# Performance work log

Hardware: AMD Instinct MI355X
Metric: run time of the kernel (lower is better)

The kernel has to match this reference:

```python
import jax, jax.numpy as jnp
import numpy as np

EPS = 1e-3   # Keras BatchNormalization default epsilon
DT = 0.2     # dt
K = 2        # PDE time steps


def _bn(x, p):
    # p: [4, C] = (gamma, beta, moving_mean, moving_var); inference-mode BN
    g, b, m, v = p
    return g * (x - m) * jax.lax.rsqrt(v + EPS) + b


def _dw(x, k):
    # depthwise 3x3 'same' conv; x: NHWC, k: (3,3,1,C)
    return jax.lax.conv_general_dilated(
        x, k, window_strides=(1, 1), padding='SAME',
        dimension_numbers=('NHWC', 'HWIO', 'NHWC'),
        feature_group_count=x.shape[-1])


def setup_inputs() -> dict:
    key = jax.random.key(0)
    ks = jax.random.split(key, 10)
    B, H, W, C = 16, 128, 128, 64
    x = jax.random.normal(ks[0], (B, H, W, C), jnp.float32)

    def kern(k):
        return jax.random.normal(k, (3, 3, 1, C), jnp.float32) * 0.1

    def bnp(k):
        k1, k2, k3, k4 = jax.random.split(k, 4)
        return jnp.stack([
            1.0 + 0.1 * jax.random.normal(k1, (C,), jnp.float32),  # gamma
            0.1 * jax.random.normal(k2, (C,), jnp.float32),        # beta
            0.1 * jax.random.normal(k3, (C,), jnp.float32),        # moving_mean
            0.5 + jax.random.uniform(k4, (C,), jnp.float32),       # moving_var > 0
        ])

    return {
        's0': x,
        'kg': kern(ks[1]), 'kg1': kern(ks[2]),
        'kDx': kern(ks[3]), 'kDy': kern(ks[4]),
        'bng': bnp(ks[5]), 'bng1': bnp(ks[6]),
        'bnDx': bnp(ks[7]), 'bnDy': bnp(ks[8]),
        'bn_out': bnp(ks[9]),
    }


def reference(s0, kg, kg1, kDx, kDy, bng, bng1, bnDx, bnDy, bn_out):
    # init_h is identity ('default' block_type); stride==1, in_chs==out_chs
    f = s0
    h = f
    h0 = f
    g = jax.nn.relu(_bn(_dw(h, kg), bng))
    g1 = jax.nn.relu(_bn(_dw(h, kg1), bng1))
    Dx = jax.nn.relu(_bn(_dw(h, kDx), bnDx))
    Dy = jax.nn.relu(_bn(_dw(h, kDy), bnDy))
    # dx = dy = 1; rolls on axis 2 and 3 exactly as in the TF code (NHWC)
    ux = 0.5 * (jnp.roll(g, 1, axis=2) - jnp.roll(g, -1, axis=2))
    vy = 0.5 * (jnp.roll(g1, 1, axis=3) - jnp.roll(g1, -1, axis=3))
    Ax = g * DT
    Ay = g1 * DT
    Bx = Dx * DT
    By = Dy * DT
    E = (ux + vy) * DT
    D = 1.0 / (1.0 + 2.0 * Bx + 2.0 * By)
    for _ in range(K):
        prev_h = h
        h = D * ((1.0 - 2.0 * Bx - 2.0 * By) * h0
                 - 2.0 * E * h
                 + (-Ax + 2.0 * Bx) * jnp.roll(h, 1, axis=2)
                 + (Ax + 2.0 * Bx) * jnp.roll(h, -1, axis=2)
                 + (-Ay + 2.0 * By) * jnp.roll(h, 1, axis=3)
                 + (Ay + 2.0 * By) * jnp.roll(h, -1, axis=3))
        h = h + D * (2.0 * DT) * f
        h0 = prev_h
    return jax.nn.relu(_bn(h, bn_out))
```

## Files before the change

### kernel.cpp

```cpp
#include <hip/hip_runtime.h>

#define HH 128
#define WW 128
#define CC 64
#define BS 512
#define RS (WW * CC)
#define NPT 4
#define NSTRIP 32
#define ROWS 8

typedef float f4 __attribute__((ext_vector_type(4)));

static __device__ __forceinline__ f4 vload(const float* p) {
    return *reinterpret_cast<const f4*>(p);
}
static __device__ __forceinline__ void vstore(float* p, f4 v) {
    *reinterpret_cast<f4*>(p) = v;
}
static __device__ __forceinline__ f4 vrelu(f4 a) {
    f4 r;
    #pragma unroll
    for (int i = 0; i < 4; ++i) r[i] = fmaxf(a[i], 0.f);
    return r;
}
static __device__ __forceinline__ f4 vrsq_eps(f4 a) {
    f4 r;
    #pragma unroll
    for (int i = 0; i < 4; ++i) r[i] = __builtin_amdgcn_rsqf(a[i] + 1e-3f);
    return r;
}
static __device__ __forceinline__ f4 vrcp(f4 a) {
    f4 r;
    #pragma unroll
    for (int i = 0; i < 4; ++i) r[i] = __builtin_amdgcn_rcpf(a[i]);
    return r;
}
static __device__ __forceinline__ void croll(f4 v, int lm, int lp, f4& cm, f4& cp) {
    const float m3 = __shfl(v.w, lm);
    const float p0 = __shfl(v.x, lp);
    cm.x = m3;  cm.y = v.x; cm.z = v.y; cm.w = v.z;
    cp.x = v.y; cp.y = v.z; cp.z = v.w; cp.w = p0;
}

static __device__ __forceinline__ void gld_lds16(const float* g, float* l) {
    __builtin_amdgcn_global_load_lds(
        (const __attribute__((address_space(1))) void*)g,
        (__attribute__((address_space(3))) void*)l,
        16, 0, 0);
}
static __device__ __forceinline__ void stage_row(const float* g, float* l,
                                                 int wv, int ln) {
    #pragma unroll
    for (int it = 0; it < 4; ++it) {
        const int off = (it * 8 + wv) * 256;
        gld_lds16(g + off + ln * 4, l + off);
    }
}

template<bool CENTER>
static __device__ __forceinline__ void conv_taps(
    const float* R, const float* WTS, int kbase, const int* oc,
    bool zl, bool zr, int c4,
    f4* ag, f4* ag1, f4* adx, f4* ady, f4* h)
{
    f4 in[6];
    #pragma unroll
    for (int jj = 0; jj < 6; ++jj) in[jj] = vload(R + oc[jj]);
    if (zl) in[0] = (f4)0.f;
    if (zr) in[5] = (f4)0.f;
    if (CENTER) {
        #pragma unroll
        for (int i = 0; i < NPT; ++i) h[i] = in[i + 1];
    }
    #pragma unroll
    for (int dw = 0; dw < 3; ++dw) {
        const int kk = kbase + dw;
        const f4 wg  = vload(WTS + (0 * 9 + kk) * CC + c4);
        const f4 wg1 = vload(WTS + (1 * 9 + kk) * CC + c4);
        const f4 wdx = vload(WTS + (2 * 9 + kk) * CC + c4);
        const f4 wdy = vload(WTS + (3 * 9 + kk) * CC + c4);
        #pragma unroll
        for (int i = 0; i < NPT; ++i) {
            ag[i]  += in[dw + i] * wg;
            ag1[i] += in[dw + i] * wg1;
            adx[i] += in[dw + i] * wdx;
            ady[i] += in[dw + i] * wdy;
        }
    }
}

__global__ __launch_bounds__(BS) void diffusion_fused(
    const float* __restrict__ s0,
    const float* __restrict__ kg,  const float* __restrict__ kg1,
    const float* __restrict__ kDx, const float* __restrict__ kDy,
    const float* __restrict__ bng,  const float* __restrict__ bng1,
    const float* __restrict__ bnDx, const float* __restrict__ bnDy,
    const float* __restrict__ bn_out,
    float* __restrict__ out)
{
    __shared__ __attribute__((aligned(16))) float ring[3][RS];
    __shared__ __attribute__((aligned(16))) float GH[2 * NSTRIP * CC];
    __shared__ __attribute__((aligned(16))) float HHb[2 * NSTRIP * CC];
    __shared__ __attribute__((aligned(16))) float WTS[4 * 9 * CC];
    __shared__ __attribute__((aligned(16))) float BNF[10 * CC];

    const int t  = threadIdx.x;
    const int cq = t & 15;
    const int c4 = cq << 2;
    const int s  = t >> 4;
    const int w0 = s << 2;
    const int l  = t & 63;
    const int wv = t >> 6;
    const int lm = (l & 48) | ((l + 15) & 15);
    const int lp = (l & 48) | ((l + 1)  & 15);
    const int sl = (s + NSTRIP - 1) & (NSTRIP - 1);
    const int sr = (s + 1) & (NSTRIP - 1);

    const int bid = blockIdx.x;
    const int img = bid >> 4;
    const int r0  = (bid & 15) << 3;
    const long imgbase = (long)img * HH * RS;

    const bool zl = (s == 0), zr = (s == NSTRIP - 1);
    int oc[6];
    oc[0] = (zl ? 0 : (w0 - 1)) * CC + c4;
    #pragma unroll
    for (int j = 1; j <= 4; ++j) oc[j] = (w0 + j - 1) * CC + c4;
    oc[5] = (zr ? (WW - 1) : (w0 + 4)) * CC + c4;
    const int wmo = ((w0 - 1) & (WW - 1)) * CC + c4;
    const int wpo = ((w0 + 4) & (WW - 1)) * CC + c4;

    if (r0 > 0)
        stage_row(s0 + imgbase + (long)(r0 - 1) * RS, ring[(r0 - 1) % 3], wv, l);
    stage_row(s0 + imgbase + (long)r0 * RS,       ring[r0 % 3],       wv, l);
    stage_row(s0 + imgbase + (long)(r0 + 1) * RS, ring[(r0 + 1) % 3], wv, l);

    {
        const float* wsrc[4] = { kg, kg1, kDx, kDy };
        #pragma unroll
        for (int base = 0; base < 576; base += BS) {
            const int slot = base + t;
            if (slot < 576) {
                const int q   = slot / 144;
                const int rem = slot - q * 144;
                const int kk  = rem >> 4;
                const int cc4 = (rem & 15) << 2;
                vstore(&WTS[(q * 9 + kk) * CC + cc4], vload(wsrc[q] + kk * CC + cc4));
            }
        }
    }
    if (s == 0) {
        #define BNF1(P, K, SC) { \
            const f4 ga = vload((P) + c4);       const f4 be = vload((P) + 64 + c4);  \
            const f4 mu = vload((P) + 128 + c4); const f4 va = vload((P) + 192 + c4); \
            const f4 sc0 = ga * vrsq_eps(va);                                         \
            vstore(&BNF[(2 * (K)) * CC + c4], sc0 * (SC));                            \
            vstore(&BNF[(2 * (K) + 1) * CC + c4], (be - mu * sc0) * (SC)); }
        BNF1(bng,    0, 1.0f);
        BNF1(bng1,   1, 1.0f);
        BNF1(bnDx,   2, 0.4f);
        BNF1(bnDy,   3, 0.4f);
        BNF1(bn_out, 4, 1.0f);
        #undef BNF1
    }
    __syncthreads();

    for (int j = 0; j < ROWS; ++j) {
        const int gr = r0 + j;
        const bool rowm = (gr > 0), rowp = (gr < HH - 1);
        const float* Rm = ring[(gr + 2) % 3];
        const float* Rc = ring[gr % 3];
        const float* Rp = ring[(gr + 1) % 3];

        f4 ag[NPT], ag1[NPT], adx[NPT], ady[NPT], h[NPT];
        #pragma unroll
        for (int i = 0; i < NPT; ++i) {
            ag[i] = (f4)0.f; ag1[i] = (f4)0.f; adx[i] = (f4)0.f; ady[i] = (f4)0.f;
        }

        if (rowm) conv_taps<false>(Rm, WTS, 0, oc, zl, zr, c4, ag, ag1, adx, ady, h);
        __syncthreads();
        if (j < ROWS - 1 && gr + 2 < HH)
            stage_row(s0 + imgbase + (long)(gr + 2) * RS, ring[(gr + 2) % 3], wv, l);

        conv_taps<true >(Rc, WTS, 3, oc, zl, zr, c4, ag, ag1, adx, ady, h);
        if (rowp) conv_taps<false>(Rp, WTS, 6, oc, zl, zr, c4, ag, ag1, adx, ady, h);

        const f4 s_g  = vload(&BNF[0 * CC + c4]), b_g  = vload(&BNF[1 * CC + c4]);
        const f4 s_g1 = vload(&BNF[2 * CC + c4]), b_g1 = vload(&BNF[3 * CC + c4]);
        const f4 s_dx = vload(&BNF[4 * CC + c4]), b_dx = vload(&BNF[5 * CC + c4]);
        const f4 s_dy = vload(&BNF[6 * CC + c4]), b_dy = vload(&BNF[7 * CC + c4]);
        f4 g[NPT], g1[NPT];
        #pragma unroll
        for (int i = 0; i < NPT; ++i) {
            g[i]  = vrelu(ag[i]  * s_g  + b_g );
            g1[i] = vrelu(ag1[i] * s_g1 + b_g1);
        }
        vstore(&GH[s * CC + c4],            g[0]);
        vstore(&GH[(NSTRIP + s) * CC + c4], g[NPT - 1]);

        f4 cWm[NPT], cWp[NPT], cCm[NPT], cCp[NPT], A0[NPT], PqD[NPT], uv[NPT];
        #pragma unroll
        for (int i = 0; i < NPT; ++i) {
            const f4 tbx = vrelu(adx[i] * s_dx + b_dx);
            const f4 tby = vrelu(ady[i] * s_dy + b_dy);
            const f4 Dv  = vrcp((f4)1.f + tbx + tby);
            const f4 Ax  = g[i]  * 0.2f;
            const f4 Ay  = g1[i] * 0.2f;
            cWm[i] = Dv * (tbx - Ax);
            cWp[i] = Dv * (tbx + Ax);
            cCm[i] = Dv * (tby - Ay);
            cCp[i] = Dv * (tby + Ay);
            A0[i]  = Dv * h[i] * ((f4)1.4f - tbx - tby);
            PqD[i] = Dv * (-0.4f);
            f4 cm, cp;
            croll(g1[i], lm, lp, cm, cp);
            uv[i] = 0.5f * (cm - cp);
        }
        uv[0] -= 0.5f * g[1];
        uv[1] += 0.5f * (g[0] - g[2]);
        uv[2] += 0.5f * (g[1] - g[3]);
        uv[3] += 0.5f * g[2];
        __syncthreads();

        f4 cE[NPT];
        {
            const f4 gL = vload(&GH[(NSTRIP + sl) * CC + c4]);
            const f4 gR = vload(&GH[sr * CC + c4]);
            cE[0] = PqD[0] * (uv[0] + 0.5f * gL);
            cE[1] = PqD[1] * uv[1];
            cE[2] = PqD[2] * uv[2];
            cE[3] = PqD[3] * (uv[3] - 0.5f * gR);
        }

        f4 hn[NPT];
        {
            const f4 hL = vload(Rc + wmo);
            const f4 hR = vload(Rc + wpo);
            #pragma unroll
            for (int i = 0; i < NPT; ++i) {
                const f4 hm = (i == 0)       ? hL : h[i - 1];
                const f4 hp = (i == NPT - 1) ? hR : h[i + 1];
                f4 cm, cp;
                croll(h[i], lm, lp, cm, cp);
                hn[i] = A0[i] + cE[i] * h[i] + cWm[i] * hm + cWp[i] * hp
                      + cCm[i] * cm + cCp[i] * cp;
            }
        }
        vstore(&HHb[s * CC + c4],            hn[0]);
        vstore(&HHb[(NSTRIP + s) * CC + c4], hn[NPT - 1]);
        __syncthreads();

        f4 h2v[NPT];
        {
            const f4 hL = vload(&HHb[(NSTRIP + sl) * CC + c4]);
            const f4 hR = vload(&HHb[sr * CC + c4]);
            #pragma unroll
            for (int i = 0; i < NPT; ++i) {
                const f4 hm = (i == 0)       ? hL : hn[i - 1];
                const f4 hp = (i == NPT - 1) ? hR : hn[i + 1];
                f4 cm, cp;
                croll(hn[i], lm, lp, cm, cp);
                h2v[i] = A0[i] + cE[i] * hn[i] + cWm[i] * hm + cWp[i] * hp
                       + cCm[i] * cm + cCp[i] * cp;
            }
        }

        const f4 s_o = vload(&BNF[8 * CC + c4]), b_o = vload(&BNF[9 * CC + c4]);
        const long rowout = imgbase + (long)gr * RS;
        #pragma unroll
        for (int i = 0; i < NPT; ++i)
            vstore(out + rowout + oc[i + 1], vrelu(h2v[i] * s_o + b_o));
    }
}

extern "C" void kernel_launch(void* const* d_in, const int* in_sizes, int n_in,
                              void* d_out, int out_size, void* d_ws, size_t ws_size,
                              hipStream_t stream) {
    const float* s0   = (const float*)d_in[0];
    const float* kg   = (const float*)d_in[1];
    const float* kg1  = (const float*)d_in[2];
    const float* kDx  = (const float*)d_in[3];
    const float* kDy  = (const float*)d_in[4];
    const float* bng  = (const float*)d_in[5];
    const float* bng1 = (const float*)d_in[6];
    const float* bnDx = (const float*)d_in[7];
    const float* bnDy = (const float*)d_in[8];
    const float* bno  = (const float*)d_in[9];
    float* out = (float*)d_out;

    dim3 grid(16 * (HH / ROWS));
    dim3 block(BS);
    diffusion_fused<<<grid, block, 0, stream>>>(
        s0, kg, kg1, kDx, kDy, bng, bng1, bnDx, bnDy, bno, out);
}
```

Baseline: 151.1 us.

## Use 4-row LDS ring, register-resident weights, and shuffle-based strip halo exchange

Grows the LDS row ring from 3 to 4 buffers so the next row's async global-to-LDS staging can start at the top of each iteration, removing one block barrier per row. The g and g1 conv weights move into registers, cutting LDS reads in the conv taps. Halo exchange between neighbouring strips now uses wave shuffles, with small LDS buffers needed only at wave boundaries. In exchange it raises register pressure from 72 extra VGPRs and uses more LDS per block, which may lower occupancy.

New measurement: 189.8 us. 1.26x slower.

```diff
diff --git a/kernel.cpp b/kernel.cpp
--- a/kernel.cpp
+++ b/kernel.cpp
@@ -41,6 +41,14 @@
     cm.x = m3;  cm.y = v.x; cm.z = v.y; cm.w = v.z;
     cp.x = v.y; cp.y = v.z; cp.z = v.w; cp.w = p0;
 }
+static __device__ __forceinline__ f4 shfl4(f4 v, int lane) {
+    f4 r;
+    r.x = __shfl(v.x, lane);
+    r.y = __shfl(v.y, lane);
+    r.z = __shfl(v.z, lane);
+    r.w = __shfl(v.w, lane);
+    return r;
+}
 
 static __device__ __forceinline__ void gld_lds16(const float* g, float* l) {
     __builtin_amdgcn_global_load_lds(
@@ -57,10 +65,10 @@
     }
 }
 
-template<bool CENTER>
+template<int KBASE, bool CENTER>
 static __device__ __forceinline__ void conv_taps(
-    const float* R, const float* WTS, int kbase, const int* oc,
-    bool zl, bool zr, int c4,
+    const float* R, const f4* wgr, const f4* wg1r, const float* WTS,
+    const int* oc, bool zl, bool zr, int c4,
     f4* ag, f4* ag1, f4* adx, f4* ady, f4* h)
 {
     f4 in[6];
@@ -74,11 +82,11 @@
     }
     #pragma unroll
     for (int dw = 0; dw < 3; ++dw) {
-        const int kk = kbase + dw;
-        const f4 wg  = vload(WTS + (0 * 9 + kk) * CC + c4);
-        const f4 wg1 = vload(WTS + (1 * 9 + kk) * CC + c4);
-        const f4 wdx = vload(WTS + (2 * 9 + kk) * CC + c4);
-        const f4 wdy = vload(WTS + (3 * 9 + kk) * CC + c4);
+        const int kk = KBASE + dw;
+        const f4 wg  = wgr[kk];
+        const f4 wg1 = wg1r[kk];
+        const f4 wdx = vload(WTS + kk * CC + c4);
+        const f4 wdy = vload(WTS + (9 + kk) * CC + c4);
         #pragma unroll
         for (int i = 0; i < NPT; ++i) {
             ag[i]  += in[dw + i] * wg;
@@ -98,10 +106,12 @@
     const float* __restrict__ bn_out,
     float* __restrict__ out)
 {
-    __shared__ __attribute__((aligned(16))) float ring[3][RS];
-    __shared__ __attribute__((aligned(16))) float GH[2 * NSTRIP * CC];
-    __shared__ __attribute__((aligned(16))) float HHb[2 * NSTRIP * CC];
-    __shared__ __attribute__((aligned(16))) float WTS[4 * 9 * CC];
+    __shared__ __attribute__((aligned(16))) float ring[4][RS];
+    __shared__ __attribute__((aligned(16))) float GHS[8 * CC];
+    __shared__ __attribute__((aligned(16))) float GHE[8 * CC];
+    __shared__ __attribute__((aligned(16))) float HBS[8 * CC];
+    __shared__ __attribute__((aligned(16))) float HBE[8 * CC];
+    __shared__ __attribute__((aligned(16))) float WTS[2 * 9 * CC];
     __shared__ __attribute__((aligned(16))) float BNF[10 * CC];
 
     const int t  = threadIdx.x;
@@ -111,10 +121,9 @@
     const int w0 = s << 2;
     const int l  = t & 63;
     const int wv = t >> 6;
+    const int jg = l >> 4;
     const int lm = (l & 48) | ((l + 15) & 15);
     const int lp = (l & 48) | ((l + 1)  & 15);
-    const int sl = (s + NSTRIP - 1) & (NSTRIP - 1);
-    const int sr = (s + 1) & (NSTRIP - 1);
 
     const int bid = blockIdx.x;
     const int img = bid >> 4;
@@ -131,23 +140,23 @@
     const int wpo = ((w0 + 4) & (WW - 1)) * CC + c4;
 
     if (r0 > 0)
-        stage_row(s0 + imgbase + (long)(r0 - 1) * RS, ring[(r0 - 1) % 3], wv, l);
-    stage_row(s0 + imgbase + (long)r0 * RS,       ring[r0 % 3],       wv, l);
-    stage_row(s0 + imgbase + (long)(r0 + 1) * RS, ring[(r0 + 1) % 3], wv, l);
-
-    {
-        const float* wsrc[4] = { kg, kg1, kDx, kDy };
-        #pragma unroll
-        for (int base = 0; base < 576; base += BS) {
-            const int slot = base + t;
-            if (slot < 576) {
-                const int q   = slot / 144;
-                const int rem = slot - q * 144;
-                const int kk  = rem >> 4;
-                const int cc4 = (rem & 15) << 2;
-                vstore(&WTS[(q * 9 + kk) * CC + cc4], vload(wsrc[q] + kk * CC + cc4));
-            }
-        }
+        stage_row(s0 + imgbase + (long)(r0 - 1) * RS, ring[(r0 - 1) & 3], wv, l);
+    stage_row(s0 + imgbase + (long)r0 * RS,       ring[r0 & 3],       wv, l);
+    stage_row(s0 + imgbase + (long)(r0 + 1) * RS, ring[(r0 + 1) & 3], wv, l);
+
+    f4 wgr[9], wg1r[9];
+    #pragma unroll
+    for (int kk = 0; kk < 9; ++kk) {
+        wgr[kk]  = vload(kg  + kk * CC + c4);
+        wg1r[kk] = vload(kg1 + kk * CC + c4);
+    }
+    if (t < 288) {
+        const int q   = (t >= 144);
+        const int rem = t - q * 144;
+        const int kk  = rem >> 4;
+        const int cc4 = (rem & 15) << 2;
+        const float* src = q ? kDy : kDx;
+        vstore(&WTS[(q * 9 + kk) * CC + cc4], vload(src + kk * CC + cc4));
     }
     if (s == 0) {
         #define BNF1(P, K, SC) { \
@@ -167,24 +176,25 @@
 
     for (int j = 0; j < ROWS; ++j) {
         const int gr = r0 + j;
+        if (j < ROWS - 1 && gr + 2 < HH)
+            stage_row(s0 + imgbase + (long)(gr + 2) * RS, ring[(gr + 2) & 3], wv, l);
+
         const bool rowm = (gr > 0), rowp = (gr < HH - 1);
-        const float* Rm = ring[(gr + 2) % 3];
-        const float* Rc = ring[gr % 3];
-        const float* Rp = ring[(gr + 1) % 3];
+        const float* Rm = ring[(gr + 3) & 3];
+        const float* Rc = ring[gr & 3];
+        const float* Rp = ring[(gr + 1) & 3];
 
         f4 ag[NPT], ag1[NPT], adx[NPT], ady[NPT], h[NPT];
         #pragma unroll
         for (int i = 0; i < NPT; ++i) {
             ag[i] = (f4)0.f; ag1[i] = (f4)0.f; adx[i] = (f4)0.f; ady[i] = (f4)0.f;
         }
-
-        if (rowm) conv_taps<false>(Rm, WTS, 0, oc, zl, zr, c4, ag, ag1, adx, ady, h);
-        __syncthreads();
-        if (j < ROWS - 1 && gr + 2 < HH)
-            stage_row(s0 + imgbase + (long)(gr + 2) * RS, ring[(gr + 2) % 3], wv, l);
-
-        conv_taps<true >(Rc, WTS, 3, oc, zl, zr, c4, ag, ag1, adx, ady, h);
-        if (rowp) conv_taps<false>(Rp, WTS, 6, oc, zl, zr, c4, ag, ag1, adx, ady, h);
+        if (rowm) conv_taps<0, false>(Rm, wgr, wg1r, WTS, oc, zl, zr, c4, ag, ag1, adx, ady, h);
+        conv_taps<3, true >(Rc, wgr, wg1r, WTS, oc, zl, zr, c4, ag, ag1, adx, ady, h);
+        if (rowp) conv_taps<6, false>(Rp, wgr, wg1r, WTS, oc, zl, zr, c4, ag, ag1, adx, ady, h);
+
+        const f4 hL = vload(Rc + wmo);
+        const f4 hR = vload(Rc + wpo);
 
         const f4 s_g  = vload(&BNF[0 * CC + c4]), b_g  = vload(&BNF[1 * CC + c4]);
         const f4 s_g1 = vload(&BNF[2 * CC + c4]), b_g1 = vload(&BNF[3 * CC + c4]);
@@ -196,8 +206,10 @@
             g[i]  = vrelu(ag[i]  * s_g  + b_g );
             g1[i] = vrelu(ag1[i] * s_g1 + b_g1);
         }
-        vstore(&GH[s * CC + c4],            g[0]);
-        vstore(&GH[(NSTRIP + s) * CC + c4], g[NPT - 1]);
+        if (jg == 0) vstore(&GHS[wv * CC + c4], g[0]);
+        if (jg == 3) vstore(&GHE[wv * CC + c4], g[3]);
+        const f4 gLs = shfl4(g[3], (l - 16) & 63);
+        const f4 gRs = shfl4(g[0], (l + 16) & 63);
 
         f4 cWm[NPT], cWp[NPT], cCm[NPT], cCp[NPT], A0[NPT], PqD[NPT], uv[NPT];
         #pragma unroll
@@ -223,47 +235,41 @@
         uv[3] += 0.5f * g[2];
         __syncthreads();
 
+        const f4 gL = (jg == 0) ? vload(&GHE[((wv + 7) & 7) * CC + c4]) : gLs;
+        const f4 gR = (jg == 3) ? vload(&GHS[((wv + 1) & 7) * CC + c4]) : gRs;
         f4 cE[NPT];
-        {
-            const f4 gL = vload(&GH[(NSTRIP + sl) * CC + c4]);
-            const f4 gR = vload(&GH[sr * CC + c4]);
-            cE[0] = PqD[0] * (uv[0] + 0.5f * gL);
-            cE[1] = PqD[1] * uv[1];
-            cE[2] = PqD[2] * uv[2];
-            cE[3] = PqD[3] * (uv[3] - 0.5f * gR);
-        }
+        cE[0] = PqD[0] * (uv[0] + 0.5f * gL);
+        cE[1] = PqD[1] * uv[1];
+        cE[2] = PqD[2] * uv[2];
+        cE[3] = PqD[3] * (uv[3] - 0.5f * gR);
 
         f4 hn[NPT];
-        {
-            const f4 hL = vload(Rc + wmo);
-            const f4 hR = vload(Rc + wpo);
-            #pragma unroll
-            for (int i = 0; i < NPT; ++i) {
-                const f4 hm = (i == 0)       ? hL : h[i - 1];
-                const f4 hp = (i == NPT - 1) ? hR : h[i + 1];
-                f4 cm, cp;
-                croll(h[i], lm, lp, cm, cp);
-                hn[i] = A0[i] + cE[i] * h[i] + cWm[i] * hm + cWp[i] * hp
-                      + cCm[i] * cm + cCp[i] * cp;
-            }
-        }
-        vstore(&HHb[s * CC + c4],            hn[0]);
-        vstore(&HHb[(NSTRIP + s) * CC + c4], hn[NPT - 1]);
+        #pragma unroll
+        for (int i = 0; i < NPT; ++i) {
+            const f4 hm = (i == 0)       ? hL : h[i - 1];
+            const f4 hp = (i == NPT - 1) ? hR : h[i + 1];
+            f4 cm, cp;
+            croll(h[i], lm, lp, cm, cp);
+            hn[i] = A0[i] + cE[i] * h[i] + cWm[i] * hm + cWp[i] * hp
+                  + cCm[i] * cm + cCp[i] * cp;
+        }
+        if (jg == 0) vstore(&HBS[wv * CC + c4], hn[0]);
+        if (jg == 3) vstore(&HBE[wv * CC + c4], hn[3]);
+        const f4 hLs = shfl4(hn[3], (l - 16) & 63);
+        const f4 hRs = shfl4(hn[0], (l + 16) & 63);
         __syncthreads();
 
+        const f4 hL2 = (jg == 0) ? vload(&HBE[((wv + 7) & 7) * CC + c4]) : hLs;
+        const f4 hR2 = (jg == 3) ? vload(&HBS[((wv + 1) & 7) * CC + c4]) : hRs;
         f4 h2v[NPT];
-        {
-            const f4 hL = vload(&HHb[(NSTRIP + sl) * CC + c4]);
-            const f4 hR = vload(&HHb[sr * CC + c4]);
-            #pragma unroll
-            for (int i = 0; i < NPT; ++i) {
-                const f4 hm = (i == 0)       ? hL : hn[i - 1];
-                const f4 hp = (i == NPT - 1) ? hR : hn[i + 1];
-                f4 cm, cp;
-                croll(hn[i], lm, lp, cm, cp);
-                h2v[i] = A0[i] + cE[i] * hn[i] + cWm[i] * hm + cWp[i] * hp
-                       + cCm[i] * cm + cCp[i] * cp;
-            }
+        #pragma unroll
+        for (int i = 0; i < NPT; ++i) {
+            const f4 hm = (i == 0)       ? hL2 : hn[i - 1];
+            const f4 hp = (i == NPT - 1) ? hR2 : hn[i + 1];
+            f4 cm, cp;
+            croll(hn[i], lm, lp, cm, cp);
+            h2v[i] = A0[i] + cE[i] * hn[i] + cWm[i] * hm + cWp[i] * hp
+                   + cCm[i] * cm + cCp[i] * cp;
         }
 
         const f4 s_o = vload(&BNF[8 * CC + c4]), b_o = vload(&BNF[9 * CC + c4]);
```
